# Performance work log

Measured on AMD Instinct MI355X. Metric: run time of the kernel, lower is better.

The kernel has to match this reference:

```python
import jax, jax.numpy as jnp
import numpy as np

EPS = 1e-5  # equinox LayerNorm default eps

def setup_inputs() -> dict:
    key = jax.random.key(0)
    k1, k2, k3, k4, k5 = jax.random.split(key, 5)
    heads, d, dH, N = 16, 1024, 64, 2048
    # lecun-normal-ish scaling for fan_in=d
    s = 1.0 / np.sqrt(d)
    return {
        "x": jax.random.normal(k1, (d, N), dtype=jnp.float32),
        "WQ": jax.random.normal(k2, (heads, d, dH), dtype=jnp.float32) * s,
        "WK": jax.random.normal(k3, (heads, d, dH), dtype=jnp.float32) * s,
        "WV": jax.random.normal(k4, (heads, d, dH), dtype=jnp.float32) * s,
        "W0": jax.random.normal(k5, (d, d), dtype=jnp.float32) * s,
    }

def reference(x, WQ, WK, WV, W0):
    # x: [d, N]
    residual = x
    # equinox LayerNorm over full shape (d, N), no affine params
    mean = jnp.mean(x)
    var = jnp.var(x)
    xn = (x - mean) * jax.lax.rsqrt(var + EPS)
    # project: [h, d_model, dH] x [d_model, N] -> [h, dH, N]
    Q = jnp.einsum('hcd,ci->hdi', WQ, xn)
    K = jnp.einsum('hcd,ci->hdi', WK, xn)
    V = jnp.einsum('hcd,ci->hdi', WV, xn)
    dH = WK.shape[-1]
    dot = jnp.einsum('hdi,hdj->hij', Q, K)  # [h, N, N]
    alpha = jax.nn.softmax(dot / jnp.sqrt(jnp.asarray(dH, dot.dtype)), axis=-1)
    attn = jnp.einsum('hij,hdj->hdi', alpha, V)  # [h, dH, N]
    N = attn.shape[2]
    attn = attn.reshape(-1, N)  # [d, N]
    out = W0 @ attn
    return out + residual
```

## Files before the change

kernel.cpp:

```cpp
#include <hip/hip_runtime.h>
#include <math.h>

typedef unsigned short u16;
typedef _Float16 f16;
typedef __attribute__((ext_vector_type(8))) short bf16x8;
typedef __attribute__((ext_vector_type(8))) unsigned short u16x8;
typedef __attribute__((ext_vector_type(4))) float f32x4;
typedef __attribute__((ext_vector_type(4))) f16 f16x4;

#define D_MODEL 1024
#define SEQ_N   2048
#define HEADS   16
#define DHEAD   64
#define M3      3072
#define JSPLIT  4
#define JCHUNK  (SEQ_N / JSPLIT)

#define GLOBAL_AS __attribute__((address_space(1)))
#define LDS_AS    __attribute__((address_space(3)))
#define ASYNC16(gp, lp) __builtin_amdgcn_global_load_lds( \
    (const GLOBAL_AS unsigned int*)(gp), (LDS_AS unsigned int*)(lp), 16, 0, 0)

__device__ __forceinline__ u16 f2bf(float f) {
  union { float f; unsigned int u; } v; v.f = f;
  unsigned int r = v.u + 0x7fffu + ((v.u >> 16) & 1u);
  return (u16)(r >> 16);
}

__global__ __launch_bounds__(256) void ln_reduce1(const float* __restrict__ x,
                                                  double* __restrict__ part, int n4) {
  const float4* x4 = (const float4*)x;
  double s = 0.0, ss = 0.0;
  for (int idx = blockIdx.x * blockDim.x + threadIdx.x; idx < n4;
       idx += gridDim.x * blockDim.x) {
    float4 v = x4[idx];
    s  += (double)v.x + (double)v.y + (double)v.z + (double)v.w;
    ss += (double)v.x * v.x + (double)v.y * v.y + (double)v.z * v.z + (double)v.w * v.w;
  }
  __shared__ double ls[256], lss[256];
  int t = threadIdx.x;
  ls[t] = s; lss[t] = ss;
  __syncthreads();
  for (int off = 128; off > 0; off >>= 1) {
    if (t < off) { ls[t] += ls[t + off]; lss[t] += lss[t + off]; }
    __syncthreads();
  }
  if (t == 0) { part[2 * blockIdx.x] = ls[0]; part[2 * blockIdx.x + 1] = lss[0]; }
}

__global__ __launch_bounds__(256) void ln_norm_t(const float* __restrict__ x,
                                                 const double* __restrict__ part,
                                                 u16* __restrict__ xnt) {
  __shared__ float tile[64][65];
  __shared__ float sstat[2];
  int t = threadIdx.x;
  {
    double* ls = (double*)&tile[0][0];
    double* lss = ls + 256;
    ls[t]  = part[2 * t] + part[2 * (t + 256)];
    lss[t] = part[2 * t + 1] + part[2 * (t + 256) + 1];
    __syncthreads();
    for (int off = 128; off > 0; off >>= 1) {
      if (t < off) { ls[t] += ls[t + off]; lss[t] += lss[t + off]; }
      __syncthreads();
    }
    if (t == 0) {
      double inv = 1.0 / ((double)D_MODEL * (double)SEQ_N);
      double mean = ls[0] * inv;
      double var  = lss[0] * inv - mean * mean;
      sstat[0] = (float)mean;
      sstat[1] = (float)(1.0 / sqrt(var + 1e-5));
    }
    __syncthreads();
  }
  float mean = sstat[0], rstd = sstat[1];
  int ib = blockIdx.x * 64, cb = blockIdx.y * 64;
  __syncthreads();
#pragma unroll
  for (int r = 0; r < 4; ++r) {
    int c = (t >> 4) + r * 16;
    int i4 = (t & 15) * 4;
    float4 v = *(const float4*)(&x[(size_t)(cb + c) * SEQ_N + ib + i4]);
    tile[c][i4 + 0] = (v.x - mean) * rstd;
    tile[c][i4 + 1] = (v.y - mean) * rstd;
    tile[c][i4 + 2] = (v.z - mean) * rstd;
    tile[c][i4 + 3] = (v.w - mean) * rstd;
  }
  __syncthreads();
#pragma unroll
  for (int r = 0; r < 2; ++r) {
    int i = (t >> 3) + r * 32;
    int c8 = (t & 7) * 8;
    u16x8 o;
#pragma unroll
    for (int j = 0; j < 8; ++j) o[j] = f2bf(tile[c8 + j][i]);
    *(u16x8*)(&xnt[(size_t)(ib + i) * D_MODEL + cb + c8]) = o;
  }
}

__global__ __launch_bounds__(256) void pack_qkv(const float* __restrict__ WQ,
                                                const float* __restrict__ WK,
                                                const float* __restrict__ WV,
                                                u16* __restrict__ Wp) {
  __shared__ float tile[32][65];
  const float* W = (blockIdx.z == 0) ? WQ : ((blockIdx.z == 1) ? WK : WV);
  int h = blockIdx.y, cb = blockIdx.x * 32;
  int t = threadIdx.x;
  int dh = t & 63, cl = t >> 6;
  for (int r = 0; r < 8; ++r) {
    int c = cl + r * 4;
    tile[c][dh] = W[((size_t)h * D_MODEL + cb + c) * DHEAD + dh];
  }
  __syncthreads();
  int c2 = t & 31, d2 = t >> 5;
  for (int r = 0; r < 8; ++r) {
    int dd = d2 + r * 8;
    Wp[(size_t)((blockIdx.z * HEADS + h) * DHEAD + dd) * D_MODEL + cb + c2] =
        f2bf(tile[c2][dd]);
  }
}

__global__ __launch_bounds__(256) void pack_w0(const float* __restrict__ W0,
                                               u16* __restrict__ W0p, int n4) {
  int idx = blockIdx.x * blockDim.x + threadIdx.x;
  if (idx >= n4) return;
  float4 v = ((const float4*)W0)[idx];
  unsigned int lo = (unsigned int)f2bf(v.x) | ((unsigned int)f2bf(v.y) << 16);
  unsigned int hi = (unsigned int)f2bf(v.z) | ((unsigned int)f2bf(v.w) << 16);
  uint2 o; o.x = lo; o.y = hi;
  *(uint2*)(&W0p[(size_t)idx * 4]) = o;
}

__global__ __launch_bounds__(256) void gemm_qkv(const u16* __restrict__ A,
                                                const u16* __restrict__ Bt,
                                                u16* __restrict__ Qt,
                                                u16* __restrict__ Kt,
                                                f16* __restrict__ Vb) {
  __shared__ __align__(16) u16 Alds[2][128 * 32];
  __shared__ __align__(16) u16 Blds[2][64 * 32];
  int t = threadIdx.x;
  int lane = t & 63, w = t >> 6;
  int g = lane >> 4, l16 = lane & 15;
  int mb = blockIdx.y * 128, nb = blockIdx.x * 64;

  f32x4 acc[2][4];
#pragma unroll
  for (int i = 0; i < 2; ++i)
#pragma unroll
    for (int j = 0; j < 4; ++j) acc[i][j] = (f32x4){0.f, 0.f, 0.f, 0.f};

  int srow = t >> 2, scol = (t & 3) * 8;
  const u16* Ag0 = A + (size_t)(mb + srow) * D_MODEL + scol;
  const u16* Ag1 = A + (size_t)(mb + 64 + srow) * D_MODEL + scol;
  const u16* Bg  = Bt + (size_t)(nb + srow) * D_MODEL + scol;

  for (int kb = 0; kb < D_MODEL; kb += 64) {
#pragma unroll
    for (int hh = 0; hh < 2; ++hh) {
      int ko = kb + hh * 32;
      ASYNC16(Ag0 + ko, &Alds[hh][t * 8]);
      ASYNC16(Ag1 + ko, &Alds[hh][2048 + t * 8]);
      ASYNC16(Bg + ko, &Blds[hh][t * 8]);
    }
    __syncthreads();
#pragma unroll
    for (int hh = 0; hh < 2; ++hh) {
      bf16x8 af[2], bf[4];
#pragma unroll
      for (int tm = 0; tm < 2; ++tm)
        af[tm] = *(const bf16x8*)(&Alds[hh][(w * 32 + tm * 16 + l16) * 32 + g * 8]);
#pragma unroll
      for (int tn = 0; tn < 4; ++tn)
        bf[tn] = *(const bf16x8*)(&Blds[hh][(tn * 16 + l16) * 32 + g * 8]);
#pragma unroll
      for (int tm = 0; tm < 2; ++tm)
#pragma unroll
        for (int tn = 0; tn < 4; ++tn)
          acc[tm][tn] = __builtin_amdgcn_mfma_f32_16x16x32_bf16(af[tm], bf[tn],
                                                                acc[tm][tn], 0, 0, 0);
    }
    __syncthreads();
  }

#pragma unroll
  for (int tm = 0; tm < 2; ++tm) {
    int row0 = mb + w * 32 + tm * 16 + g * 4;
#pragma unroll
    for (int tn = 0; tn < 4; ++tn) {
      int col = nb + tn * 16 + l16;
      if (mb < 2 * D_MODEL) {
        u16* T = (mb < D_MODEL) ? Qt : Kt;
        int rbase = (mb < D_MODEL) ? row0 : row0 - D_MODEL;
        ushort4 o;
        o.x = f2bf(acc[tm][tn][0]); o.y = f2bf(acc[tm][tn][1]);
        o.z = f2bf(acc[tm][tn][2]); o.w = f2bf(acc[tm][tn][3]);
        *(ushort4*)(&T[(size_t)col * D_MODEL + rbase]) = o;
      } else {
        int rbase = row0 - 2 * D_MODEL;
#pragma unroll
        for (int r = 0; r < 4; ++r)
          Vb[(size_t)(rbase + r) * SEQ_N + col] = (f16)acc[tm][tn][r];
      }
    }
  }
}

__global__ __launch_bounds__(256) void gemm_bf16(const u16* __restrict__ A,
                                                 const u16* __restrict__ Bt,
                                                 float* __restrict__ C,
                                                 const float* __restrict__ res,
                                                 int M, int N, int K) {
  __shared__ __align__(16) u16 Alds[2][64 * 32];
  __shared__ __align__(16) u16 Blds[2][64 * 32];
  int t = threadIdx.x;
  int w = t >> 6, lane = t & 63;
  int g = lane >> 4, l16 = lane & 15;
  int mb = blockIdx.y * 64, nb = blockIdx.x * 64;
  f32x4 acc[4];
  for (int i = 0; i < 4; ++i) acc[i] = (f32x4){0.f, 0.f, 0.f, 0.f};
  int srow = t >> 2, scol = (t & 3) * 8;
  const u16* Ag = A + (size_t)(mb + srow) * K + scol;
  const u16* Bg = Bt + (size_t)(nb + srow) * K + scol;
  for (int kb = 0; kb < K; kb += 64) {
#pragma unroll
    for (int hh = 0; hh < 2; ++hh) {
      int ko = kb + hh * 32;
      ASYNC16(Ag + ko, &Alds[hh][t * 8]);
      ASYNC16(Bg + ko, &Blds[hh][t * 8]);
    }
    __syncthreads();
#pragma unroll
    for (int hh = 0; hh < 2; ++hh) {
      bf16x8 af = *(const bf16x8*)(&Alds[hh][(w * 16 + l16) * 32 + g * 8]);
#pragma unroll
      for (int tn = 0; tn < 4; ++tn) {
        bf16x8 bf = *(const bf16x8*)(&Blds[hh][(tn * 16 + l16) * 32 + g * 8]);
        acc[tn] = __builtin_amdgcn_mfma_f32_16x16x32_bf16(af, bf, acc[tn], 0, 0, 0);
      }
    }
    __syncthreads();
  }
  int col0 = nb + l16;
  int row0 = mb + w * 16 + g * 4;
#pragma unroll
  for (int tn = 0; tn < 4; ++tn) {
    int col = col0 + tn * 16;
#pragma unroll
    for (int r = 0; r < 4; ++r) {
      int row = row0 + r;
      float v = acc[tn][r];
      if (res) v += res[(size_t)row * N + col];
      C[(size_t)row * N + col] = v;
    }
  }
}

__global__ __launch_bounds__(256, 8) void attn_mfma(const u16* __restrict__ Qt,
                                                    const u16* __restrict__ Kt,
                                                    const f16* __restrict__ Vb,
                                                    f16* __restrict__ Opart,
                                                    float* __restrict__ Lpart) {
  __shared__ __align__(16) u16 Klds[64][72];
  __shared__ __align__(16) f16 Vlds[64][72];
  int h = blockIdx.y;
  int ib = blockIdx.x * 64;
  int sp = blockIdx.z;
  int j0 = sp * JCHUNK;
  int t = threadIdx.x;
  int w = t >> 6, lane = t & 63;
  int g = lane >> 4, l16 = lane & 15;

  bf16x8 bq[2];
  {
    const u16* qb = Qt + (size_t)(ib + w * 16 + l16) * D_MODEL + h * DHEAD + g * 8;
    bq[0] = *(const bf16x8*)(qb);
    bq[1] = *(const bf16x8*)(qb + 32);
  }

  f32x4 acc_o[4];
#pragma unroll
  for (int i = 0; i < 4; ++i) acc_o[i] = (f32x4){0.f, 0.f, 0.f, 0.f};
  float lsum = 0.f;

  int srow = t >> 3, sch = (t & 7) * 8;
  for (int it = 0; it < JCHUNK / 64; ++it) {
    int jb = j0 + it * 64;
    uint4 kr0 = *(const uint4*)(&Kt[(size_t)(jb + srow) * D_MODEL + h * DHEAD + sch]);
    uint4 kr1 = *(const uint4*)(&Kt[(size_t)(jb + srow + 32) * D_MODEL + h * DHEAD + sch]);
    uint4 vr0 = *(const uint4*)(&Vb[(size_t)(h * DHEAD + srow) * SEQ_N + jb + sch]);
    uint4 vr1 = *(const uint4*)(&Vb[(size_t)(h * DHEAD + srow + 32) * SEQ_N + jb + sch]);
    *(uint4*)(&Klds[srow][sch]) = kr0;
    *(uint4*)(&Klds[srow + 32][sch]) = kr1;
    *(uint4*)(&Vlds[srow][sch]) = vr0;
    *(uint4*)(&Vlds[srow + 32][sch]) = vr1;
    __syncthreads();

    f32x4 s[4];
#pragma unroll
    for (int i = 0; i < 4; ++i) s[i] = (f32x4){0.f, 0.f, 0.f, 0.f};
#pragma unroll
    for (int kk = 0; kk < 2; ++kk)
#pragma unroll
      for (int tn = 0; tn < 4; ++tn) {
        bf16x8 ak = *(const bf16x8*)(&Klds[tn * 16 + l16][kk * 32 + g * 8]);
        s[tn] = __builtin_amdgcn_mfma_f32_16x16x32_bf16(ak, bq[kk], s[tn], 0, 0, 0);
      }
    f16x4 pf[4];
#pragma unroll
    for (int tn = 0; tn < 4; ++tn)
#pragma unroll
      for (int r = 0; r < 4; ++r) {
        float pv = exp2f(fmaf(s[tn][r], 0.18033688f, -5.7707801f));
        lsum += pv;
        pf[tn][r] = (f16)pv;
      }
#pragma unroll
    for (int tn = 0; tn < 4; ++tn)
#pragma unroll
      for (int td = 0; td < 4; ++td) {
        f16x4 bv = *(const f16x4*)(&Vlds[td * 16 + l16][tn * 16 + g * 4]);
        acc_o[td] =
            __builtin_amdgcn_mfma_f32_16x16x16f16(pf[tn], bv, acc_o[td], 0, 0, 0);
      }
    __syncthreads();
  }

  lsum += __shfl_xor(lsum, 16, 64);
  lsum += __shfl_xor(lsum, 32, 64);
  if (g == 0)
    Lpart[((size_t)sp * HEADS + h) * SEQ_N + ib + w * 16 + l16] = lsum;

#pragma unroll
  for (int td = 0; td < 4; ++td) {
    int dh = h * DHEAD + td * 16 + l16;
#pragma unroll
    for (int r = 0; r < 4; ++r) {
      int i = ib + w * 16 + g * 4 + r;
      Opart[((size_t)sp * SEQ_N + i) * D_MODEL + dh] = (f16)acc_o[td][r];
    }
  }
}

__global__ __launch_bounds__(256) void attn_combine(const f16* __restrict__ Opart,
                                                    const float* __restrict__ Lpart,
                                                    u16* __restrict__ attnt) {
  int i = blockIdx.x;
  int c = threadIdx.x * 4;
  int h = c >> 6;
  float l = 0.f;
#pragma unroll
  for (int s = 0; s < JSPLIT; ++s) l += Lpart[((size_t)s * HEADS + h) * SEQ_N + i];
  float o[4] = {0.f, 0.f, 0.f, 0.f};
#pragma unroll
  for (int s = 0; s < JSPLIT; ++s) {
    f16x4 v = *(const f16x4*)(&Opart[((size_t)s * SEQ_N + i) * D_MODEL + c]);
#pragma unroll
    for (int r = 0; r < 4; ++r) o[r] += (float)v[r];
  }
  float inv = 1.0f / l;
  ushort4 ob;
  ob.x = f2bf(o[0] * inv); ob.y = f2bf(o[1] * inv);
  ob.z = f2bf(o[2] * inv); ob.w = f2bf(o[3] * inv);
  *(ushort4*)(&attnt[(size_t)i * D_MODEL + c]) = ob;
}

extern "C" void kernel_launch(void* const* d_in, const int* in_sizes, int n_in,
                              void* d_out, int out_size, void* d_ws, size_t ws_size,
                              hipStream_t stream) {
  const float* x  = (const float*)d_in[0];
  const float* WQ = (const float*)d_in[1];
  const float* WK = (const float*)d_in[2];
  const float* WV = (const float*)d_in[3];
  const float* W0 = (const float*)d_in[4];
  float* out = (float*)d_out;

  char* ws = (char*)d_ws;
  size_t off = 0;
  double* part  = (double*)(ws + off); off += 8192;
  u16*    xnt   = (u16*)(ws + off); off += (size_t)SEQ_N * D_MODEL * 2;
  u16*    Wp    = (u16*)(ws + off); off += (size_t)M3 * D_MODEL * 2;
  u16*    W0p   = (u16*)(ws + off); off += (size_t)D_MODEL * D_MODEL * 2;
  u16*    Qt    = (u16*)(ws + off); off += (size_t)SEQ_N * D_MODEL * 2;
  u16*    Kt    = (u16*)(ws + off); off += (size_t)SEQ_N * D_MODEL * 2;
  f16*    Vb    = (f16*)(ws + off); off += (size_t)D_MODEL * SEQ_N * 2;
  u16*    attnt = (u16*)(ws + off); off += (size_t)SEQ_N * D_MODEL * 2;
  f16*    Opart = (f16*)(ws + off); off += (size_t)JSPLIT * SEQ_N * D_MODEL * 2;
  float*  Lpart = (float*)(ws + off); off += (size_t)JSPLIT * HEADS * SEQ_N * 4;

  ln_reduce1<<<512, 256, 0, stream>>>(x, part, (D_MODEL * SEQ_N) / 4);
  ln_norm_t<<<dim3(SEQ_N / 64, D_MODEL / 64), 256, 0, stream>>>(x, part, xnt);
  pack_qkv<<<dim3(D_MODEL / 32, HEADS, 3), 256, 0, stream>>>(WQ, WK, WV, Wp);
  pack_w0<<<(D_MODEL * D_MODEL / 4 + 255) / 256, 256, 0, stream>>>(W0, W0p,
                                                                   D_MODEL * D_MODEL / 4);
  gemm_qkv<<<dim3(SEQ_N / 64, M3 / 128), 256, 0, stream>>>(Wp, xnt, Qt, Kt, Vb);
  attn_mfma<<<dim3(SEQ_N / 64, HEADS, JSPLIT), 256, 0, stream>>>(Qt, Kt, Vb, Opart, Lpart);
  attn_combine<<<SEQ_N, 256, 0, stream>>>(Opart, Lpart, attnt);
  gemm_bf16<<<dim3(SEQ_N / 64, D_MODEL / 64), 256, 0, stream>>>(W0p, attnt, out, x,
                                                                D_MODEL, SEQ_N, D_MODEL);
}
```

Measured before the change: 183.4 us.

## Remap attention grid for XCD-local K/V reuse and shrink GEMM K-step

The attention launch becomes a 1-D grid of 2048 blocks, and the block index is decoded so that blocks sharing a (head, split) combo land on the same XCD. Since consecutive blocks are dispatched round-robin across the 8 XCDs, this is meant to keep K/V tiles in the local L2. Both GEMM kernels drop their 64-wide K step (two 32-wide LDS stages per barrier) in favour of one 32-wide stage per iteration. That halves LDS use but doubles the number of barriers and load round-trips, which may reduce latency hiding.

```diff
diff --git a/kernel.cpp b/kernel.cpp
--- a/kernel.cpp
+++ b/kernel.cpp
@@ -136,8 +136,8 @@
                                                 u16* __restrict__ Qt,
                                                 u16* __restrict__ Kt,
                                                 f16* __restrict__ Vb) {
-  __shared__ __align__(16) u16 Alds[2][128 * 32];
-  __shared__ __align__(16) u16 Blds[2][64 * 32];
+  __shared__ __align__(16) u16 Alds[128 * 32];
+  __shared__ __align__(16) u16 Blds[64 * 32];
   int t = threadIdx.x;
   int lane = t & 63, w = t >> 6;
   int g = lane >> 4, l16 = lane & 15;
@@ -154,31 +154,24 @@
   const u16* Ag1 = A + (size_t)(mb + 64 + srow) * D_MODEL + scol;
   const u16* Bg  = Bt + (size_t)(nb + srow) * D_MODEL + scol;
 
-  for (int kb = 0; kb < D_MODEL; kb += 64) {
-#pragma unroll
-    for (int hh = 0; hh < 2; ++hh) {
-      int ko = kb + hh * 32;
-      ASYNC16(Ag0 + ko, &Alds[hh][t * 8]);
-      ASYNC16(Ag1 + ko, &Alds[hh][2048 + t * 8]);
-      ASYNC16(Bg + ko, &Blds[hh][t * 8]);
-    }
-    __syncthreads();
-#pragma unroll
-    for (int hh = 0; hh < 2; ++hh) {
-      bf16x8 af[2], bf[4];
-#pragma unroll
-      for (int tm = 0; tm < 2; ++tm)
-        af[tm] = *(const bf16x8*)(&Alds[hh][(w * 32 + tm * 16 + l16) * 32 + g * 8]);
+  for (int kb = 0; kb < D_MODEL; kb += 32) {
+    ASYNC16(Ag0 + kb, &Alds[t * 8]);
+    ASYNC16(Ag1 + kb, &Alds[2048 + t * 8]);
+    ASYNC16(Bg + kb, &Blds[t * 8]);
+    __syncthreads();
+    bf16x8 af[2], bf[4];
+#pragma unroll
+    for (int tm = 0; tm < 2; ++tm)
+      af[tm] = *(const bf16x8*)(&Alds[(w * 32 + tm * 16 + l16) * 32 + g * 8]);
+#pragma unroll
+    for (int tn = 0; tn < 4; ++tn)
+      bf[tn] = *(const bf16x8*)(&Blds[(tn * 16 + l16) * 32 + g * 8]);
+#pragma unroll
+    for (int tm = 0; tm < 2; ++tm)
 #pragma unroll
       for (int tn = 0; tn < 4; ++tn)
-        bf[tn] = *(const bf16x8*)(&Blds[hh][(tn * 16 + l16) * 32 + g * 8]);
-#pragma unroll
-      for (int tm = 0; tm < 2; ++tm)
-#pragma unroll
-        for (int tn = 0; tn < 4; ++tn)
-          acc[tm][tn] = __builtin_amdgcn_mfma_f32_16x16x32_bf16(af[tm], bf[tn],
-                                                                acc[tm][tn], 0, 0, 0);
-    }
+        acc[tm][tn] = __builtin_amdgcn_mfma_f32_16x16x32_bf16(af[tm], bf[tn],
+                                                              acc[tm][tn], 0, 0, 0);
     __syncthreads();
   }
 
@@ -210,8 +203,8 @@
                                                  float* __restrict__ C,
                                                  const float* __restrict__ res,
                                                  int M, int N, int K) {
-  __shared__ __align__(16) u16 Alds[2][64 * 32];
-  __shared__ __align__(16) u16 Blds[2][64 * 32];
+  __shared__ __align__(16) u16 Alds[64 * 32];
+  __shared__ __align__(16) u16 Blds[64 * 32];
   int t = threadIdx.x;
   int w = t >> 6, lane = t & 63;
   int g = lane >> 4, l16 = lane & 15;
@@ -221,22 +214,15 @@
   int srow = t >> 2, scol = (t & 3) * 8;
   const u16* Ag = A + (size_t)(mb + srow) * K + scol;
   const u16* Bg = Bt + (size_t)(nb + srow) * K + scol;
-  for (int kb = 0; kb < K; kb += 64) {
-#pragma unroll
-    for (int hh = 0; hh < 2; ++hh) {
-      int ko = kb + hh * 32;
-      ASYNC16(Ag + ko, &Alds[hh][t * 8]);
-      ASYNC16(Bg + ko, &Blds[hh][t * 8]);
-    }
-    __syncthreads();
-#pragma unroll
-    for (int hh = 0; hh < 2; ++hh) {
-      bf16x8 af = *(const bf16x8*)(&Alds[hh][(w * 16 + l16) * 32 + g * 8]);
-#pragma unroll
-      for (int tn = 0; tn < 4; ++tn) {
-        bf16x8 bf = *(const bf16x8*)(&Blds[hh][(tn * 16 + l16) * 32 + g * 8]);
-        acc[tn] = __builtin_amdgcn_mfma_f32_16x16x32_bf16(af, bf, acc[tn], 0, 0, 0);
-      }
+  for (int kb = 0; kb < K; kb += 32) {
+    ASYNC16(Ag + kb, &Alds[t * 8]);
+    ASYNC16(Bg + kb, &Blds[t * 8]);
+    __syncthreads();
+    bf16x8 af = *(const bf16x8*)(&Alds[(w * 16 + l16) * 32 + g * 8]);
+#pragma unroll
+    for (int tn = 0; tn < 4; ++tn) {
+      bf16x8 bf = *(const bf16x8*)(&Blds[(tn * 16 + l16) * 32 + g * 8]);
+      acc[tn] = __builtin_amdgcn_mfma_f32_16x16x32_bf16(af, bf, acc[tn], 0, 0, 0);
     }
     __syncthreads();
   }
@@ -262,9 +248,13 @@
                                                     float* __restrict__ Lpart) {
   __shared__ __align__(16) u16 Klds[64][72];
   __shared__ __align__(16) f16 Vlds[64][72];
-  int h = blockIdx.y;
-  int ib = blockIdx.x * 64;
-  int sp = blockIdx.z;
+  int b = blockIdx.x;
+  int xcd = b & 7, slot = b >> 3;
+  int combo = xcd * 8 + (slot >> 5);
+  int qt = slot & 31;
+  int h = combo & 15;
+  int sp = combo >> 4;
+  int ib = qt * 64;
   int j0 = sp * JCHUNK;
   int t = threadIdx.x;
   int w = t >> 6, lane = t & 63;
@@ -393,7 +383,7 @@
   pack_w0<<<(D_MODEL * D_MODEL / 4 + 255) / 256, 256, 0, stream>>>(W0, W0p,
                                                                    D_MODEL * D_MODEL / 4);
   gemm_qkv<<<dim3(SEQ_N / 64, M3 / 128), 256, 0, stream>>>(Wp, xnt, Qt, Kt, Vb);
-  attn_mfma<<<dim3(SEQ_N / 64, HEADS, JSPLIT), 256, 0, stream>>>(Qt, Kt, Vb, Opart, Lpart);
+  attn_mfma<<<2048, 256, 0, stream>>>(Qt, Kt, Vb, Opart, Lpart);
   attn_combine<<<SEQ_N, 256, 0, stream>>>(Opart, Lpart, attnt);
   gemm_bf16<<<dim3(SEQ_N / 64, D_MODEL / 64), 256, 0, stream>>>(W0p, attnt, out, x,
                                                                 D_MODEL, SEQ_N, D_MODEL);
```

Result: no change. 183.6 us (+0.1%).
